# Kernel tuning notes

Measured on AMD Instinct MI355X. Metric: run time of the kernel, lower is better.

The kernel has to match this reference:

```python
import jax, jax.numpy as jnp
import numpy as np

R, S = 3, 2  # scale factor r/s = 1.5, kernel k = s+1 = 3


def _make_bilinear_weight(r, s):
    # Faithful port of fill_weights_BiLinear, flattened to [r^2, 1, k, k]
    k = s + 1
    w = np.zeros((r * r, 1, k, k), dtype=np.float64)
    a = s / r / 2
    nn = np.linspace(0, s - a, r)
    ny, nx = np.meshgrid(nn, nn)
    for i, (x, y) in enumerate(zip(nx.flatten(), ny.flatten())):
        x0, x1 = int(np.floor(x)), int(np.ceil(x))
        y0, y1 = int(np.floor(y)), int(np.ceil(y))
        if x1 == x0:
            x1 += 1
        if y1 == y0:
            y1 += 1
        w[i, 0, x0, y0] += (x1 - x) * (y1 - y)
        w[i, 0, x0, min(y1, k - 1)] += (x1 - x) * (y - y0)
        w[i, 0, min(x1, k - 1), y0] += (x - x0) * (y1 - y)
        w[i, 0, min(x1, k - 1), min(y1, k - 1)] += (x - x0) * (y - y0)
    return jnp.asarray(w, dtype=jnp.float32)


def setup_inputs() -> dict:
    key = jax.random.key(0)
    inp = jax.random.normal(key, (4, 512, 512, 32), dtype=jnp.float32)
    weight = _make_bilinear_weight(R, S)
    return {"input": inp, "weight": weight}


def reference(input, weight) -> jnp.ndarray:
    r, s = R, S
    k = s + 1
    pad = k // 2 - 1 if k % 2 == 0 else k // 2  # compute_padding
    B, H, W, C = input.shape
    x = jnp.transpose(input, (0, 3, 1, 2))  # [B, C, H, W]
    x = jnp.pad(x, ((0, 0), (0, 0), (pad, pad), (pad, pad)), mode="edge")  # replicate pad
    # conv3d with depth-1 kernel == per-channel 2D conv: fold C into batch
    x = x.reshape(B * C, 1, H + 2 * pad, W + 2 * pad)
    y = jax.lax.conv_general_dilated(
        x, weight, window_strides=(s, s), padding="VALID",
        dimension_numbers=("NCHW", "OIHW", "NCHW"),
    )  # [B*C, r^2, H/s, W/s]
    Hs, Ws = y.shape[-2], y.shape[-1]
    # permute(0,2,1,3,4) + PixelShuffle(r) + squeeze: depth-to-space over r^2 channel
    y = y.reshape(B, C, r, r, Hs, Ws)
    y = jnp.transpose(y, (0, 1, 4, 2, 5, 3)).reshape(B, C, Hs * r, Ws * r)
    return jnp.transpose(y, (0, 2, 3, 1))  # back to channels-last [B, H', W', C]
```

## Files before the change

kernel.cpp:

```cpp
#include <hip/hip_runtime.h>


constexpr int B = 4, H = 512, W = 512, C = 32;
constexpr int HS = 256, WS = 256;
constexpr int HO = 768, WO = 768;

__global__ __launch_bounds__(256) void fracscale_kernel(
    const float* __restrict__ in, const float* __restrict__ wgt,
    float* __restrict__ out)
{
    __shared__ float w[81];
    if (threadIdx.x < 81) w[threadIdx.x] = wgt[threadIdx.x];
    __syncthreads();

    unsigned u = blockIdx.x * 256u + threadIdx.x;
    const int cg = u & 7;
    const int ws = (u >> 3) & 255;
    const int hs = (u >> 11) & 255;
    const int b  = u >> 19;

    int iy[3], ix[3];
#pragma unroll
    for (int d = 0; d < 3; ++d) {
        int y = 2 * hs + d - 1;
        iy[d] = y < 0 ? 0 : (y > H - 1 ? H - 1 : y);
        int x = 2 * ws + d - 1;
        ix[d] = x < 0 ? 0 : (x > W - 1 ? W - 1 : x);
    }

    const float* inb = in + (size_t)b * H * W * C + (size_t)cg * 4;

    float4 acc[3][3];
#pragma unroll
    for (int ra = 0; ra < 3; ++ra)
#pragma unroll
        for (int rb = 0; rb < 3; ++rb)
            acc[ra][rb] = make_float4(0.f, 0.f, 0.f, 0.f);

#pragma unroll
    for (int dy = 0; dy < 3; ++dy) {
        float4 v[3];
#pragma unroll
        for (int dx = 0; dx < 3; ++dx) {
            v[dx] = *(const float4*)(inb + ((size_t)iy[dy] * W + ix[dx]) * C);
        }
#pragma unroll
        for (int ra = 0; ra < 3; ++ra)
#pragma unroll
            for (int rb = 0; rb < 3; ++rb) {
#pragma unroll
                for (int dx = 0; dx < 3; ++dx) {
                    const float wv = w[(ra * 3 + rb) * 9 + dy * 3 + dx];
                    acc[ra][rb].x = fmaf(wv, v[dx].x, acc[ra][rb].x);
                    acc[ra][rb].y = fmaf(wv, v[dx].y, acc[ra][rb].y);
                    acc[ra][rb].z = fmaf(wv, v[dx].z, acc[ra][rb].z);
                    acc[ra][rb].w = fmaf(wv, v[dx].w, acc[ra][rb].w);
                }
            }
    }

    float* outb = out + (size_t)b * HO * WO * C + (size_t)cg * 4;
#pragma unroll
    for (int ra = 0; ra < 3; ++ra)
#pragma unroll
        for (int rb = 0; rb < 3; ++rb) {
            const int ho = hs * 3 + ra;
            const int wo = ws * 3 + rb;
            *(float4*)(outb + ((size_t)ho * WO + wo) * C) = acc[ra][rb];
        }
}

extern "C" void kernel_launch(void* const* d_in, const int* in_sizes, int n_in,
                              void* d_out, int out_size, void* d_ws, size_t ws_size,
                              hipStream_t stream) {
    const float* in  = (const float*)d_in[0];
    const float* wgt = (const float*)d_in[1];
    float* out = (float*)d_out;

    const int total = B * HS * WS * 8;
    const int blocks = total / 256;
    fracscale_kernel<<<blocks, 256, 0, stream>>>(in, wgt, out);
}
```

Before: 82.87 us.

## Exploit separable bilinear weights and use nontemporal output stores

```diff
diff --git a/kernel.cpp b/kernel.cpp
--- a/kernel.cpp
+++ b/kernel.cpp
@@ -2,16 +2,20 @@
 
 
 constexpr int B = 4, H = 512, W = 512, C = 32;
-constexpr int HS = 256, WS = 256;
 constexpr int HO = 768, WO = 768;
+
+typedef float f32x4 __attribute__((ext_vector_type(4)));
 
 __global__ __launch_bounds__(256) void fracscale_kernel(
     const float* __restrict__ in, const float* __restrict__ wgt,
     float* __restrict__ out)
 {
-    __shared__ float w[81];
-    if (threadIdx.x < 81) w[threadIdx.x] = wgt[threadIdx.x];
-    __syncthreads();
+    float G[3][3];
+#pragma unroll
+    for (int p = 0; p < 3; ++p)
+#pragma unroll
+        for (int t = 0; t < 3; ++t)
+            G[p][t] = wgt[27 * p + 3 * t];
 
     unsigned u = blockIdx.x * 256u + threadIdx.x;
     const int cg = u & 7;
@@ -30,44 +34,47 @@
 
     const float* inb = in + (size_t)b * H * W * C + (size_t)cg * 4;
 
-    float4 acc[3][3];
+    f32x4 acc[3][3];
 #pragma unroll
     for (int ra = 0; ra < 3; ++ra)
 #pragma unroll
         for (int rb = 0; rb < 3; ++rb)
-            acc[ra][rb] = make_float4(0.f, 0.f, 0.f, 0.f);
+            acc[ra][rb] = (f32x4)(0.f);
 
 #pragma unroll
     for (int dy = 0; dy < 3; ++dy) {
-        float4 v[3];
+        f32x4 v[3];
 #pragma unroll
-        for (int dx = 0; dx < 3; ++dx) {
-            v[dx] = *(const float4*)(inb + ((size_t)iy[dy] * W + ix[dx]) * C);
+        for (int dx = 0; dx < 3; ++dx)
+            v[dx] = *(const f32x4*)(inb + ((size_t)iy[dy] * W + ix[dx]) * C);
+
+        f32x4 r[3];
+#pragma unroll
+        for (int rb = 0; rb < 3; ++rb) {
+            r[rb] = G[rb][0] * v[0];
+            r[rb] += G[rb][1] * v[1];
+            r[rb] += G[rb][2] * v[2];
         }
 #pragma unroll
-        for (int ra = 0; ra < 3; ++ra)
+        for (int ra = 0; ra < 3; ++ra) {
+            const float wv = G[ra][dy];
 #pragma unroll
-            for (int rb = 0; rb < 3; ++rb) {
-#pragma unroll
-                for (int dx = 0; dx < 3; ++dx) {
-                    const float wv = w[(ra * 3 + rb) * 9 + dy * 3 + dx];
-                    acc[ra][rb].x = fmaf(wv, v[dx].x, acc[ra][rb].x);
-                    acc[ra][rb].y = fmaf(wv, v[dx].y, acc[ra][rb].y);
-                    acc[ra][rb].z = fmaf(wv, v[dx].z, acc[ra][rb].z);
-                    acc[ra][rb].w = fmaf(wv, v[dx].w, acc[ra][rb].w);
-                }
-            }
+            for (int rb = 0; rb < 3; ++rb)
+                acc[ra][rb] += wv * r[rb];
+        }
     }
 
     float* outb = out + (size_t)b * HO * WO * C + (size_t)cg * 4;
 #pragma unroll
-    for (int ra = 0; ra < 3; ++ra)
+    for (int ra = 0; ra < 3; ++ra) {
+        const int ho = hs * 3 + ra;
 #pragma unroll
         for (int rb = 0; rb < 3; ++rb) {
-            const int ho = hs * 3 + ra;
             const int wo = ws * 3 + rb;
-            *(float4*)(outb + ((size_t)ho * WO + wo) * C) = acc[ra][rb];
+            __builtin_nontemporal_store(acc[ra][rb],
+                (f32x4*)(outb + ((size_t)ho * WO + wo) * C));
         }
+    }
 }
 
 extern "C" void kernel_launch(void* const* d_in, const int* in_sizes, int n_in,
@@ -77,7 +84,6 @@
     const float* wgt = (const float*)d_in[1];
     float* out = (float*)d_out;
 
-    const int total = B * HS * WS * 8;
-    const int blocks = total / 256;
-    fracscale_kernel<<<blocks, 256, 0, stream>>>(in, wgt, out);
+    const int total = B * 256 * 256 * 8;
+    fracscale_kernel<<<total / 256, 256, 0, stream>>>(in, wgt, out);
 }
```

Result: faster. 67.24 us (-18.9%).
